# Performance work log

Measured on AMD Instinct MI355X. Metric: run time of the kernel, lower is better.

Reference implementation:

```python
import jax, jax.numpy as jnp
import numpy as np

P, N = 12000, 100          # pillars, max points per pillar
C_IN, C_OUT = 9, 32        # 4 raw + 3 cluster + 2 center -> units = 64 // 2
EPS = 1e-3                 # BatchNorm eps from change_default_args


def setup_inputs() -> dict:
    key = jax.random.key(0)
    ks = jax.random.split(key, 12)
    shp = (1, 1, P, N)
    pillar_x = jax.random.normal(ks[0], shp) * 10.0
    pillar_y = jax.random.normal(ks[1], shp) * 10.0
    pillar_z = jax.random.normal(ks[2], shp)
    pillar_i = jax.random.uniform(ks[3], shp)
    num_voxels = jax.random.randint(ks[4], (P,), 1, N + 1).astype(jnp.int32)
    x_sub_shaped = jax.random.normal(ks[5], shp) * 10.0
    y_sub_shaped = jax.random.normal(ks[6], shp) * 10.0
    # valid-point mask: first num_voxels[p] slots are 1
    mask = (jnp.arange(N)[None, None, None, :] < num_voxels[None, None, :, None]).astype(jnp.float32)
    # PFNLayer params: Linear(9,32,bias=False) + BatchNorm2d(32) in eval mode
    W = jax.random.normal(ks[7], (C_OUT, C_IN)) * 0.1
    gamma = jax.random.uniform(ks[8], (C_OUT,), minval=0.5, maxval=1.5)
    beta = jax.random.normal(ks[9], (C_OUT,)) * 0.1
    bn_mean = jax.random.normal(ks[10], (C_OUT,)) * 0.1
    bn_var = jax.random.uniform(ks[11], (C_OUT,), minval=0.5, maxval=1.5)
    return {
        "pillar_x": pillar_x, "pillar_y": pillar_y, "pillar_z": pillar_z,
        "pillar_i": pillar_i, "num_voxels": num_voxels,
        "x_sub_shaped": x_sub_shaped, "y_sub_shaped": y_sub_shaped,
        "mask": mask, "W": W, "gamma": gamma, "beta": beta,
        "bn_mean": bn_mean, "bn_var": bn_var,
    }


def reference(pillar_x, pillar_y, pillar_z, pillar_i, num_voxels,
              x_sub_shaped, y_sub_shaped, mask, W, gamma, beta,
              bn_mean, bn_var):
    # ---- PillarFeatureNet feature assembly ----
    pillar_xyz = jnp.concatenate([pillar_x, pillar_y, pillar_z], axis=1)  # [1,3,P,N]
    nv = num_voxels.astype(pillar_x.dtype).reshape(1, 1, P, 1)
    points_mean = jnp.sum(pillar_xyz, axis=3, keepdims=True) / nv        # [1,3,P,1]
    f_cluster = pillar_xyz - points_mean                                  # [1,3,P,N]
    f_center = jnp.concatenate([pillar_x - x_sub_shaped,
                                pillar_y - y_sub_shaped], axis=1)        # [1,2,P,N]
    features = jnp.concatenate(
        [pillar_x, pillar_y, pillar_z, pillar_i, f_cluster, f_center], axis=1)  # [1,9,P,N]
    masked = (features * mask).transpose(0, 2, 3, 1)                     # [1,P,N,9]
    # ---- PFNLayer 0: Linear + BN (eval) + ReLU + max + repeat-concat ----
    x = jnp.einsum('bpnc,uc->bpnu', masked, W)                           # [1,P,N,32]
    inv_std = jax.lax.rsqrt(bn_var + EPS)
    x = (x - bn_mean) * (inv_std * gamma) + beta
    x = jax.nn.relu(x)
    x_max = jnp.max(x, axis=2, keepdims=True)                            # [1,P,1,32]
    x_repeat = jnp.broadcast_to(x_max, x.shape)                          # [1,P,N,32]
    return jnp.concatenate([x, x_repeat], axis=3)                        # [1,P,N,64]
```

## Files before the change

### kernel.cpp

```cpp
#include <hip/hip_runtime.h>

#define NPIL 12000
#define NPTS 100
#define CIN 9
#define COUT 32

__launch_bounds__(256, 4)
__global__ void pfn_kernel(const float* __restrict__ px, const float* __restrict__ py,
                           const float* __restrict__ pz, const float* __restrict__ pi,
                           const int*   __restrict__ nvox,
                           const float* __restrict__ xs, const float* __restrict__ ys,
                           const float* __restrict__ mk,
                           const float* __restrict__ W,  const float* __restrict__ gma,
                           const float* __restrict__ bta, const float* __restrict__ bmean,
                           const float* __restrict__ bvar,
                           float* __restrict__ out) {
    __shared__ float lin[7][NPTS];
    __shared__ float lxo[NPTS * COUT];
    __shared__ float lmean[3];
    __shared__ int   lmax[COUT];

    const int p = blockIdx.x;
    const int t = threadIdx.x;

    const float* srcs[7] = {px, py, pz, pi, xs, ys, mk};
    for (int j = t; j < 7 * NPTS; j += 256) {
        int a = j / NPTS;
        int n = j - a * NPTS;
        lin[a][n] = srcs[a][p * NPTS + n];
    }
    if (t < COUT) lmax[t] = 0;
    __syncthreads();

    if (t < 96) {
        int c = t >> 5, j = t & 31;
        float v = lin[c][j] + lin[c][j + 32] + lin[c][j + 64];
        if (j < 4) v += lin[c][j + 96];
        v += __shfl_xor(v, 16);
        v += __shfl_xor(v, 8);
        v += __shfl_xor(v, 4);
        v += __shfl_xor(v, 2);
        v += __shfl_xor(v, 1);
        if (j == 0) lmean[c] = v / (float)nvox[p];
    }

    const int u = t & 31;
    const float s  = rsqrtf(bvar[u] + 1e-3f) * gma[u];
    const float b  = bta[u] - bmean[u] * s;
    const float w0 = W[u * CIN + 0] * s, w1 = W[u * CIN + 1] * s, w2 = W[u * CIN + 2] * s;
    const float w3 = W[u * CIN + 3] * s, w4 = W[u * CIN + 4] * s, w5 = W[u * CIN + 5] * s;
    const float w6 = W[u * CIN + 6] * s, w7 = W[u * CIN + 7] * s, w8 = W[u * CIN + 8] * s;
    __syncthreads();

    const float mx = lmean[0], my = lmean[1], mz = lmean[2];
    float vmax = 0.f;
    for (int n = (t >> 5); n < NPTS; n += 8) {
        float x  = lin[0][n], y = lin[1][n], z = lin[2][n], it = lin[3][n];
        float fx = x - lin[4][n], fy = y - lin[5][n];
        float m  = lin[6][n];
        float dot = x * w0 + y * w1 + z * w2 + it * w3
                  + (x - mx) * w4 + (y - my) * w5 + (z - mz) * w6
                  + fx * w7 + fy * w8;
        float v = fmaxf(fmaf(m, dot, b), 0.f);
        lxo[n * COUT + u] = v;
        vmax = fmaxf(vmax, v);
    }
    atomicMax(&lmax[u], __float_as_int(vmax));
    __syncthreads();

    const float4* lxo4  = (const float4*)lxo;
    const float4* lmax4 = (const float4*)lmax;
    float4* out4 = (float4*)(out + (size_t)p * (NPTS * 64));
    for (int idx = t; idx < NPTS * 16; idx += 256) {
        int n = idx >> 4;
        int q = idx & 15;
        float4 v = (q < 8) ? lxo4[n * 8 + q] : lmax4[q - 8];
        out4[idx] = v;
    }
}

extern "C" void kernel_launch(void* const* d_in, const int* in_sizes, int n_in,
                              void* d_out, int out_size, void* d_ws, size_t ws_size,
                              hipStream_t stream) {
    const float* px  = (const float*)d_in[0];
    const float* py  = (const float*)d_in[1];
    const float* pz  = (const float*)d_in[2];
    const float* pi  = (const float*)d_in[3];
    const int*   nv  = (const int*)  d_in[4];
    const float* xs  = (const float*)d_in[5];
    const float* ys  = (const float*)d_in[6];
    const float* mk  = (const float*)d_in[7];
    const float* W   = (const float*)d_in[8];
    const float* gma = (const float*)d_in[9];
    const float* bta = (const float*)d_in[10];
    const float* bmn = (const float*)d_in[11];
    const float* bvr = (const float*)d_in[12];
    float* out = (float*)d_out;

    pfn_kernel<<<dim3(NPIL), dim3(256), 0, stream>>>(
        px, py, pz, pi, nv, xs, ys, mk, W, gma, bta, bmn, bvr, out);
}
```

Measured before the change: 361.8 us.

## Write linear outputs directly to global and pack inputs point-major in LDS

The per-point Linear+BN+ReLU results now go straight to global memory instead of being staged in a 12.8KB shared buffer and copied out. The max half is written in a separate float4 loop. Inputs are stored point-major in an 8-wide shared array so each point's features load as two float4 reads, and the staging loop drops its integer division. Less shared memory per block should raise occupancy, at the cost of 32-float scalar global stores per point row instead of fully vectorised float4 row writes.

```diff
diff --git a/kernel.cpp b/kernel.cpp
--- a/kernel.cpp
+++ b/kernel.cpp
@@ -15,33 +15,32 @@
                            const float* __restrict__ bta, const float* __restrict__ bmean,
                            const float* __restrict__ bvar,
                            float* __restrict__ out) {
-    __shared__ float lin[7][NPTS];
-    __shared__ float lxo[NPTS * COUT];
+    __shared__ float lin8[NPTS][8];
     __shared__ float lmean[3];
     __shared__ int   lmax[COUT];
 
     const int p = blockIdx.x;
     const int t = threadIdx.x;
+    const float fnv = (float)nvox[p];
 
-    const float* srcs[7] = {px, py, pz, pi, xs, ys, mk};
-    for (int j = t; j < 7 * NPTS; j += 256) {
-        int a = j / NPTS;
-        int n = j - a * NPTS;
-        lin[a][n] = srcs[a][p * NPTS + n];
+    if (t < NPTS) {
+        const size_t o = (size_t)p * NPTS + t;
+        lin8[t][0] = px[o]; lin8[t][1] = py[o]; lin8[t][2] = pz[o]; lin8[t][3] = pi[o];
+        lin8[t][4] = xs[o]; lin8[t][5] = ys[o]; lin8[t][6] = mk[o];
     }
-    if (t < COUT) lmax[t] = 0;
+    if (t >= 224) lmax[t - 224] = 0;
     __syncthreads();
 
     if (t < 96) {
         int c = t >> 5, j = t & 31;
-        float v = lin[c][j] + lin[c][j + 32] + lin[c][j + 64];
-        if (j < 4) v += lin[c][j + 96];
+        float v = lin8[j][c] + lin8[j + 32][c] + lin8[j + 64][c];
+        if (j < 4) v += lin8[j + 96][c];
         v += __shfl_xor(v, 16);
         v += __shfl_xor(v, 8);
         v += __shfl_xor(v, 4);
         v += __shfl_xor(v, 2);
         v += __shfl_xor(v, 1);
-        if (j == 0) lmean[c] = v / (float)nvox[p];
+        if (j == 0) lmean[c] = v / fnv;
     }
 
     const int u = t & 31;
@@ -53,29 +52,25 @@
     __syncthreads();
 
     const float mx = lmean[0], my = lmean[1], mz = lmean[2];
+    float* outp = out + (size_t)p * (NPTS * 64);
     float vmax = 0.f;
     for (int n = (t >> 5); n < NPTS; n += 8) {
-        float x  = lin[0][n], y = lin[1][n], z = lin[2][n], it = lin[3][n];
-        float fx = x - lin[4][n], fy = y - lin[5][n];
-        float m  = lin[6][n];
-        float dot = x * w0 + y * w1 + z * w2 + it * w3
-                  + (x - mx) * w4 + (y - my) * w5 + (z - mz) * w6
-                  + fx * w7 + fy * w8;
-        float v = fmaxf(fmaf(m, dot, b), 0.f);
-        lxo[n * COUT + u] = v;
+        float4 a = *(const float4*)&lin8[n][0];
+        float4 c4 = *(const float4*)&lin8[n][4];
+        float dot = a.x * w0 + a.y * w1 + a.z * w2 + a.w * w3
+                  + (a.x - mx) * w4 + (a.y - my) * w5 + (a.z - mz) * w6
+                  + (a.x - c4.x) * w7 + (a.y - c4.y) * w8;
+        float v = fmaxf(fmaf(c4.z, dot, b), 0.f);
+        outp[n * 64 + u] = v;
         vmax = fmaxf(vmax, v);
     }
     atomicMax(&lmax[u], __float_as_int(vmax));
     __syncthreads();
 
-    const float4* lxo4  = (const float4*)lxo;
     const float4* lmax4 = (const float4*)lmax;
-    float4* out4 = (float4*)(out + (size_t)p * (NPTS * 64));
-    for (int idx = t; idx < NPTS * 16; idx += 256) {
-        int n = idx >> 4;
-        int q = idx & 15;
-        float4 v = (q < 8) ? lxo4[n * 8 + q] : lmax4[q - 8];
-        out4[idx] = v;
+    for (int idx = t; idx < NPTS * 8; idx += 256) {
+        int n = idx >> 3, q = idx & 7;
+        ((float4*)(outp + n * 64 + 32))[q] = lmax4[q];
     }
 }
 
```

Result: no change. 364.1 us (+0.6%).
